# Kernel optimization log

Measured on AMD Instinct MI355X. Metric: run time of the kernel, lower is better.

## Reference

```python
import jax, jax.numpy as jnp
import numpy as np

DIM = 1024
HEADS = 16
HEAD_DIM = DIM // HEADS
EPS = 1e-6


def rmsnorm(x, w):
    var = jnp.mean(x * x, axis=-1, keepdims=True)
    return x * jax.lax.rsqrt(var + EPS) * w


def setup_inputs() -> dict:
    key = jax.random.key(0)
    ks = jax.random.split(key, 8)
    B, N, M = 2, 2048, 512
    s = 1.0 / np.sqrt(DIM)
    return {
        "x": jax.random.normal(ks[0], (B, N, DIM), jnp.float32),
        "context": jax.random.normal(ks[1], (B, M, DIM), jnp.float32),
        "qkv_w": jax.random.normal(ks[2], (3 * DIM, DIM), jnp.float32) * s,
        "kv_y_w": jax.random.normal(ks[3], (2 * DIM, DIM), jnp.float32) * s,
        "proj_w": jax.random.normal(ks[4], (DIM, DIM), jnp.float32) * s,
        "proj_b": jnp.zeros((DIM,), jnp.float32),
        "q_norm_w": jnp.ones((HEAD_DIM,), jnp.float32),
        "k_norm_w": jnp.ones((HEAD_DIM,), jnp.float32),
    }


def reference(x, context, qkv_w, kv_y_w, proj_w, proj_b, q_norm_w, k_norm_w):
    B, N, C = x.shape
    H, D = HEADS, HEAD_DIM
    scale = D ** -0.5
    qkv = (x @ qkv_w.T).reshape(B, N, 3, H, D).transpose(2, 0, 3, 1, 4)
    q, kx, vx = qkv[0], qkv[1], qkv[2]
    q = rmsnorm(q, q_norm_w)
    kx = rmsnorm(kx, k_norm_w)
    M = context.shape[1]
    kv = (context @ kv_y_w.T).reshape(B, M, 2, H, D).transpose(2, 0, 3, 1, 4)
    ky, vy = kv[0], kv[1]
    ky = rmsnorm(ky, k_norm_w)
    k = jnp.concatenate([kx, ky], axis=2)  # [B,H,N+M,D]
    v = jnp.concatenate([vx, vy], axis=2)
    attn = jax.nn.softmax(jnp.einsum("bhnd,bhmd->bhnm", q, k) * scale, axis=-1)
    out = jnp.einsum("bhnm,bhmd->bhnd", attn, v).transpose(0, 2, 1, 3).reshape(B, N, C)
    return out @ proj_w.T + proj_b
```

## Files before the change

### kernel.cpp

```cpp
#include <hip/hip_runtime.h>
#include <hip/hip_bf16.h>
#include <stdint.h>

#define DEVINL __device__ __forceinline__

typedef unsigned short u16;
typedef unsigned int u32;
typedef __attribute__((ext_vector_type(8))) __bf16 bf16x8;
typedef __attribute__((ext_vector_type(4))) float f32x4;
typedef __attribute__((ext_vector_type(16))) float f32x16;

static constexpr int NQ = 2048, MC = 512, DIMC = 1024, LTOT = 2560;
static constexpr float EPS = 1e-6f;

DEVINL u16 f2bf(float f) {
  u32 u = __float_as_uint(f);
  u32 r = (u + 0x7FFFu + ((u >> 16) & 1u)) >> 16;
  return (u16)r;
}
DEVINL float bf2f(u16 h) { return __uint_as_float(((u32)h) << 16); }

DEVINL void gload16(const void* g, void* l) {
  __builtin_amdgcn_global_load_lds((const __attribute__((address_space(1))) void*)g,
                                   (__attribute__((address_space(3))) void*)l, 16, 0, 0);
}

__global__ void cvt_all(const float* __restrict__ x, const float* __restrict__ ctx,
                        const float* __restrict__ w1, const float* __restrict__ w2,
                        const float* __restrict__ w3,
                        u16* __restrict__ xb, u16* __restrict__ cb, u16* __restrict__ wq,
                        u16* __restrict__ wk, u16* __restrict__ wp) {
  const int bk = blockIdx.x;
  const float* src; u16* dst; int lb;
  if (bk < 2048)      { src = x;   dst = xb; lb = bk; }
  else if (bk < 2560) { src = ctx; dst = cb; lb = bk - 2048; }
  else if (bk < 4096) { src = w1;  dst = wq; lb = bk - 2560; }
  else if (bk < 5120) { src = w2;  dst = wk; lb = bk - 4096; }
  else                { src = w3;  dst = wp; lb = bk - 5120; }
  size_t i = ((size_t)lb * 256 + threadIdx.x) * 8;
  float4 a = *(const float4*)(src + i);
  float4 b = *(const float4*)(src + i + 4);
  union { uint4 u; u16 s[8]; } o;
  o.s[0] = f2bf(a.x); o.s[1] = f2bf(a.y); o.s[2] = f2bf(a.z); o.s[3] = f2bf(a.w);
  o.s[4] = f2bf(b.x); o.s[5] = f2bf(b.y); o.s[6] = f2bf(b.z); o.s[7] = f2bf(b.w);
  *(uint4*)(dst + i) = o.u;
}

template <int M, int N, int K, bool OUT_BF16, bool HAS_BIAS>
__launch_bounds__(256, 2)
__global__ void gemm_bt(const u16* __restrict__ A, const u16* __restrict__ Bw,
                        void* __restrict__ Cout, const float* __restrict__ bias) {
  __shared__ u16 la[128 * 64];
  __shared__ u16 lb[128 * 64];
  const int tid = threadIdx.x;
  const int lane = tid & 63, wid = tid >> 6;
  const int tm = blockIdx.x / (N / 128), tn = blockIdx.x % (N / 128);
  const int m0 = tm * 128, n0 = tn * 128;
  const int wm = (wid >> 1) * 64, wn = (wid & 1) * 64;
  const int srow = lane >> 3, scol = (lane & 7) * 8;
  const int cn = lane & 15, rg = lane >> 4;

  f32x4 acc[4][4] = {};

  for (int kt = 0; kt < K; kt += 64) {
    __syncthreads();
#pragma unroll
    for (int c = 0; c < 4; ++c) {
      int s = c * 4 + wid;
      gload16(A + (size_t)(m0 + s * 8 + srow) * K + kt + scol, &la[s * 512]);
      gload16(Bw + (size_t)(n0 + s * 8 + srow) * K + kt + scol, &lb[s * 512]);
    }
    __syncthreads();
#pragma unroll
    for (int kk = 0; kk < 2; ++kk) {
      bf16x8 af[4], bfr[4];
      const int ko = kk * 32 + rg * 8;
#pragma unroll
      for (int mi = 0; mi < 4; ++mi) af[mi] = *(const bf16x8*)&la[(wm + mi * 16 + cn) * 64 + ko];
#pragma unroll
      for (int ni = 0; ni < 4; ++ni) bfr[ni] = *(const bf16x8*)&lb[(wn + ni * 16 + cn) * 64 + ko];
#pragma unroll
      for (int mi = 0; mi < 4; ++mi)
#pragma unroll
        for (int ni = 0; ni < 4; ++ni)
          acc[mi][ni] = __builtin_amdgcn_mfma_f32_16x16x32_bf16(af[mi], bfr[ni], acc[mi][ni], 0, 0, 0);
    }
  }
#pragma unroll
  for (int mi = 0; mi < 4; ++mi)
#pragma unroll
    for (int ni = 0; ni < 4; ++ni) {
      const int col = n0 + wn + ni * 16 + cn;
      const float bv = HAS_BIAS ? bias[col] : 0.0f;
#pragma unroll
      for (int r = 0; r < 4; ++r) {
        const int row = m0 + wm + mi * 16 + rg * 4 + r;
        const float v = acc[mi][ni][r] + bv;
        if (OUT_BF16) ((u16*)Cout)[(size_t)row * N + col] = f2bf(v);
        else          ((float*)Cout)[(size_t)row * N + col] = v;
      }
    }
}

__global__ void reorg_kv(const u16* __restrict__ qkvx, const u16* __restrict__ kvy,
                         const float* __restrict__ knw,
                         u16* __restrict__ kfb, u16* __restrict__ vfb) {
  __shared__ u16 lk[64 * 72];
  const int tid = threadIdx.x;
  const int bh = blockIdx.x / 40, g = blockIdx.x % 40;
  const int b = bh >> 4, h = bh & 15;
  const u16* src; int stride, kcol, vcol, srow0;
  if (g < 32) {
    src = qkvx; stride = 3 * DIMC; kcol = DIMC + h * 64; vcol = 2 * DIMC + h * 64;
    srow0 = b * NQ + g * 64;
  } else {
    src = kvy; stride = 2 * DIMC; kcol = h * 64; vcol = DIMC + h * 64;
    srow0 = b * MC + (g - 32) * 64;
  }
  {
    const int i = tid >> 2, d0 = (tid & 3) * 16;
    const u16* p = src + (size_t)(srow0 + i) * stride + kcol + d0;
    uint4 r0 = *(const uint4*)(p);
    uint4 r1 = *(const uint4*)(p + 8);
    const u16* s0 = (const u16*)&r0; const u16* s1 = (const u16*)&r1;
    float f[16]; float ss = 0.f;
#pragma unroll
    for (int j = 0; j < 8; ++j) { f[j] = bf2f(s0[j]); ss += f[j] * f[j]; }
#pragma unroll
    for (int j = 0; j < 8; ++j) { f[8 + j] = bf2f(s1[j]); ss += f[8 + j] * f[8 + j]; }
    ss += __shfl_xor(ss, 1); ss += __shfl_xor(ss, 2);
    const float rs = rsqrtf(ss * (1.0f / 64.0f) + EPS);
    union { uint4 u; u16 s[8]; } o0, o1;
#pragma unroll
    for (int j = 0; j < 8; ++j) o0.s[j] = f2bf(f[j] * rs * knw[d0 + j]);
#pragma unroll
    for (int j = 0; j < 8; ++j) o1.s[j] = f2bf(f[8 + j] * rs * knw[d0 + 8 + j]);
    *(uint4*)&lk[i * 72 + d0] = o0.u;
    *(uint4*)&lk[i * 72 + d0 + 8] = o1.u;
  }
  __syncthreads();
#pragma unroll
  for (int c0 = 0; c0 < 512; c0 += 256) {
    const int c = c0 + tid;
    const int l = c & 63, s = (c >> 6) & 3, tt = c >> 8;
    const int ln32 = l & 31, hi = l >> 5;
    const size_t tbase = ((size_t)bh * 80 + g * 2 + tt) * 2048;
    uint4 kv4 = *(const uint4*)&lk[(tt * 32 + ln32) * 72 + s * 16 + hi * 8];
    *(uint4*)(kfb + tbase + s * 512 + l * 8) = kv4;
    const int key = tt * 32 + (s & 1) * 16 + hi * 8;
    const int d = (s >> 1) * 32 + ln32;
    const u16* vp = src + (size_t)(srow0 + key) * stride + vcol + d;
    union { uint4 u; u16 e[8]; } t;
#pragma unroll
    for (int j = 0; j < 8; ++j) t.e[j] = vp[(size_t)j * stride];
    *(uint4*)(vfb + tbase + s * 512 + l * 8) = t.u;
  }
}

__launch_bounds__(256, 4)
__global__ void attn_fwd(const u16* __restrict__ qkvx, const u16* __restrict__ kfb,
                         const u16* __restrict__ vfb, const float* __restrict__ qnw,
                         u16* __restrict__ pacc, float* __restrict__ mlb) {
  const int tid = threadIdx.x;
  const int lane = tid & 63, wid = tid >> 6;
  const int hi = lane >> 5, ln32 = lane & 31;
  const int swz = (blockIdx.x & 7) * 128 + (blockIdx.x >> 3);
  const int sp = swz & 1, qt = (swz >> 1) & 15, bh = swz >> 5;
  const int b = bh >> 4, h = bh & 15;
  const int qrow = qt * 128 + wid * 32 + ln32;

  union U4 { uint4 u; bf16x8 v; };

  bf16x8 qb[4];
  {
    const u16* qp = qkvx + (size_t)(b * NQ + qrow) * (3 * DIMC) + h * 64 + hi * 8;
    uint4 qr4[4];
#pragma unroll
    for (int s = 0; s < 4; ++s) qr4[s] = *(const uint4*)(qp + s * 16);
    float f[32]; float ss = 0.f;
#pragma unroll
    for (int s = 0; s < 4; ++s) {
      const u16* e = (const u16*)&qr4[s];
#pragma unroll
      for (int j = 0; j < 8; ++j) { float v = bf2f(e[j]); f[s * 8 + j] = v; ss += v * v; }
    }
    ss += __shfl_xor(ss, 32);
    const float rs = rsqrtf(ss * (1.0f / 64.0f) + EPS) * 0.125f * 1.44269504088896f;
#pragma unroll
    for (int s = 0; s < 4; ++s) {
      union { u16 s16[8]; bf16x8 v; } o;
#pragma unroll
      for (int j = 0; j < 8; ++j) o.s16[j] = f2bf(f[s * 8 + j] * rs * qnw[s * 16 + hi * 8 + j]);
      qb[s] = o.v;
    }
  }

  const u16* kbase = kfb + ((size_t)bh * 80 + sp * 40) * 2048 + lane * 8;
  const u16* vbase = vfb + ((size_t)bh * 80 + sp * 40) * 2048 + lane * 8;

  U4 kf[4];
#pragma unroll
  for (int s = 0; s < 4; ++s) kf[s].u = *(const uint4*)(kbase + s * 512);

  float m_run = -1e30f, l_run = 0.f;
  f32x16 acc0 = {}, acc1 = {};

#pragma unroll 2
  for (int t = 0; t < 40; ++t) {
    const u16* vt = vbase + (size_t)t * 2048;
    U4 vf[4];
#pragma unroll
    for (int vi = 0; vi < 4; ++vi) vf[vi].u = *(const uint4*)(vt + vi * 512);

    f32x16 sa = {};
#pragma unroll
    for (int s = 0; s < 4; ++s)
      sa = __builtin_amdgcn_mfma_f32_32x32x16_bf16(kf[s].v, qb[s], sa, 0, 0, 0);

    const u16* kt = kbase + (size_t)(t + 1) * 2048;
    U4 kn[4];
#pragma unroll
    for (int s = 0; s < 4; ++s) kn[s].u = *(const uint4*)(kt + s * 512);

    float t8[8];
#pragma unroll
    for (int j = 0; j < 8; ++j) t8[j] = fmaxf(sa[j], sa[j + 8]);
    float t4m[4];
#pragma unroll
    for (int j = 0; j < 4; ++j) t4m[j] = fmaxf(t8[j], t8[j + 4]);
    float mx = fmaxf(fmaxf(t4m[0], t4m[2]), fmaxf(t4m[1], t4m[3]));
    mx = fmaxf(mx, __shfl_xor(mx, 32));
    if (__any(mx > m_run + 8.0f)) {
      const float mn = fmaxf(m_run, mx);
      const float corr = exp2f(m_run - mn);
      m_run = mn;
      l_run *= corr;
#pragma unroll
      for (int r = 0; r < 16; ++r) {
        const int qr = (r & 3) + 8 * (r >> 2) + 4 * hi;
        const float c = __shfl(corr, qr);
        acc0[r] *= c; acc1[r] *= c;
      }
    }
    float p[16];
#pragma unroll
    for (int r = 0; r < 16; ++r) p[r] = exp2f(sa[r] - m_run);
    float s8[8];
#pragma unroll
    for (int j = 0; j < 8; ++j) s8[j] = p[j] + p[j + 8];
    float s4[4];
#pragma unroll
    for (int j = 0; j < 4; ++j) s4[j] = s8[j] + s8[j + 4];
    float sum = (s4[0] + s4[2]) + (s4[1] + s4[3]);
    sum += __shfl_xor(sum, 32);
    l_run += sum;

    u32 w[8];
#pragma unroll
    for (int j = 0; j < 8; ++j) {
      __hip_bfloat162 h2 = __float22bfloat162_rn(make_float2(p[2 * j], p[2 * j + 1]));
      w[j] = *(u32*)&h2;
    }
    union { u32 w4[4]; bf16x8 v; } pa0, pa1;
#pragma unroll
    for (int g = 0; g < 2; ++g)
#pragma unroll
      for (int j = 0; j < 2; ++j) {
        const u32 a = w[4 * g + j], c = w[4 * g + j + 2];
        const u32 xa = __shfl_xor(a, 32), xc = __shfl_xor(c, 32);
        u32 lo_w = hi ? xc : a;
        u32 hi_w = hi ? c : xa;
        if (g == 0) { pa0.w4[j] = lo_w; pa0.w4[j + 2] = hi_w; }
        else        { pa1.w4[j] = lo_w; pa1.w4[j + 2] = hi_w; }
      }

    acc0 = __builtin_amdgcn_mfma_f32_32x32x16_bf16(pa0.v, vf[0].v, acc0, 0, 0, 0);
    acc0 = __builtin_amdgcn_mfma_f32_32x32x16_bf16(pa1.v, vf[1].v, acc0, 0, 0, 0);
    acc1 = __builtin_amdgcn_mfma_f32_32x32x16_bf16(pa0.v, vf[2].v, acc1, 0, 0, 0);
    acc1 = __builtin_amdgcn_mfma_f32_32x32x16_bf16(pa1.v, vf[3].v, acc1, 0, 0, 0);

#pragma unroll
    for (int s = 0; s < 4; ++s) kf[s] = kn[s];
  }

  const float rinv = 1.0f / l_run;
  u16* po = pacc + (size_t)sp * 4194304 +
            (size_t)(b * NQ + qt * 128 + wid * 32) * DIMC + h * 64 + ln32;
#pragma unroll
  for (int r = 0; r < 16; ++r) {
    const int qr = (r & 3) + 8 * (r >> 2) + 4 * hi;
    const float ri = __shfl(rinv, qr);
    po[(size_t)qr * DIMC] = f2bf(acc0[r] * ri);
    po[(size_t)qr * DIMC + 32] = f2bf(acc1[r] * ri);
  }
  if (lane < 32) {
    const int mlidx = (b * NQ + qt * 128 + wid * 32 + ln32) * 16 + h;
    mlb[(sp * 2 + 0) * 65536 + mlidx] = m_run;
    mlb[(sp * 2 + 1) * 65536 + mlidx] = l_run;
  }
}

__global__ void attn_combine(const u16* __restrict__ pacc, const float* __restrict__ mlb,
                             u16* __restrict__ attnb) {
  const int g = blockIdx.x * 256 + threadIdx.x;
  const int combo = g >> 3, dc = (g & 7) * 8;
  const float m0 = mlb[combo],             l0 = mlb[65536 + combo];
  const float m1 = mlb[2 * 65536 + combo], l1 = mlb[3 * 65536 + combo];
  const float m = fmaxf(m0, m1);
  const float w0 = l0 * exp2f(m0 - m), w1 = l1 * exp2f(m1 - m);
  const float rinv = 1.0f / (w0 + w1);
  const int row = combo >> 4, h = combo & 15;
  const size_t off = (size_t)row * DIMC + h * 64 + dc;
  uint4 a0 = *(const uint4*)(pacc + off);
  uint4 a1 = *(const uint4*)(pacc + 4194304 + off);
  const u16* p0 = (const u16*)&a0; const u16* p1 = (const u16*)&a1;
  union { uint4 u; u16 s[8]; } o;
#pragma unroll
  for (int j = 0; j < 8; ++j)
    o.s[j] = f2bf((w0 * bf2f(p0[j]) + w1 * bf2f(p1[j])) * rinv);
  *(uint4*)(attnb + off) = o.u;
}

extern "C" void kernel_launch(void* const* d_in, const int* in_sizes, int n_in,
                              void* d_out, int out_size, void* d_ws, size_t ws_size,
                              hipStream_t stream) {
  const float* x      = (const float*)d_in[0];
  const float* ctx    = (const float*)d_in[1];
  const float* qkv_w  = (const float*)d_in[2];
  const float* kv_y_w = (const float*)d_in[3];
  const float* proj_w = (const float*)d_in[4];
  const float* proj_b = (const float*)d_in[5];
  const float* q_norm_w = (const float*)d_in[6];
  const float* k_norm_w = (const float*)d_in[7];
  float* out = (float*)d_out;

  char* ws = (char*)d_ws;
  u16* xb    = (u16*)(ws);
  u16* cb    = (u16*)(ws + 8388608);
  u16* wqkv  = (u16*)(ws + 10485760);
  u16* wkv   = (u16*)(ws + 16777216);
  u16* wproj = (u16*)(ws + 20971520);
  u16* qkvx  = (u16*)(ws + 23068672);
  u16* kvy   = (u16*)(ws + 48234496);
  u16* kfb   = (u16*)(ws + 52428800);
  u16* vfb   = (u16*)(ws + 62914560);
  u16* attnb = (u16*)(ws + 73400320);
  u16*   pacc = (u16*)(ws);
  float* mlb  = (float*)(ws + 16777216);

  cvt_all<<<5632, 256, 0, stream>>>(x, ctx, qkv_w, kv_y_w, proj_w, xb, cb, wqkv, wkv, wproj);

  gemm_bt<4096, 3072, 1024, true, false><<<32 * 24, 256, 0, stream>>>(xb, wqkv, qkvx, nullptr);
  gemm_bt<1024, 2048, 1024, true, false><<<8 * 16, 256, 0, stream>>>(cb, wkv, kvy, nullptr);
  reorg_kv<<<32 * 40, 256, 0, stream>>>(qkvx, kvy, k_norm_w, kfb, vfb);
  attn_fwd<<<1024, 256, 0, stream>>>(qkvx, kfb, vfb, q_norm_w, pacc, mlb);
  attn_combine<<<2048, 256, 0, stream>>>(pacc, mlb, attnb);
  gemm_bt<4096, 1024, 1024, false, true><<<32 * 8, 256, 0, stream>>>(attnb, wproj, out, proj_b);
}
```

Before: 271.4 us.

## Add BM-templated GEMM tiles and restructure attention inner loop with MFMA row sums

The GEMM is templated on its M tile size so the small KV-context GEMM and the output projection run with 64-row tiles, launching more blocks to fill the GPU. The attention loop is reworked in several ways: K fragments double-buffer without copies, the max reduction is flattened, and the cross-half P shuffle uses v_permlane32_swap. MFMA sections are given raised s_setprio priority. The softmax denominator is now accumulated by an extra MFMA against a vector of ones instead of scalar adds and shuffles, which adds matrix work and bf16-rounded row sums in exchange for fewer VALU ops.

```diff
diff --git a/kernel.cpp b/kernel.cpp
--- a/kernel.cpp
+++ b/kernel.cpp
@@ -46,48 +46,53 @@
   *(uint4*)(dst + i) = o.u;
 }
 
-template <int M, int N, int K, bool OUT_BF16, bool HAS_BIAS>
+template <int BM, int M, int N, int K, bool OUT_BF16, bool HAS_BIAS>
 __launch_bounds__(256, 2)
 __global__ void gemm_bt(const u16* __restrict__ A, const u16* __restrict__ Bw,
                         void* __restrict__ Cout, const float* __restrict__ bias) {
-  __shared__ u16 la[128 * 64];
+  constexpr int MI = BM / 32;
+  __shared__ u16 la[BM * 64];
   __shared__ u16 lb[128 * 64];
   const int tid = threadIdx.x;
   const int lane = tid & 63, wid = tid >> 6;
   const int tm = blockIdx.x / (N / 128), tn = blockIdx.x % (N / 128);
-  const int m0 = tm * 128, n0 = tn * 128;
-  const int wm = (wid >> 1) * 64, wn = (wid & 1) * 64;
+  const int m0 = tm * BM, n0 = tn * 128;
+  const int wm = (wid >> 1) * (BM / 2), wn = (wid & 1) * 64;
   const int srow = lane >> 3, scol = (lane & 7) * 8;
   const int cn = lane & 15, rg = lane >> 4;
 
-  f32x4 acc[4][4] = {};
+  f32x4 acc[MI][4] = {};
 
   for (int kt = 0; kt < K; kt += 64) {
     __syncthreads();
 #pragma unroll
+    for (int c = 0; c < MI; ++c) {
+      int s = c * 4 + wid;
+      gload16(A + (size_t)(m0 + s * 8 + srow) * K + kt + scol, &la[s * 512]);
+    }
+#pragma unroll
     for (int c = 0; c < 4; ++c) {
       int s = c * 4 + wid;
-      gload16(A + (size_t)(m0 + s * 8 + srow) * K + kt + scol, &la[s * 512]);
       gload16(Bw + (size_t)(n0 + s * 8 + srow) * K + kt + scol, &lb[s * 512]);
     }
     __syncthreads();
 #pragma unroll
     for (int kk = 0; kk < 2; ++kk) {
-      bf16x8 af[4], bfr[4];
+      bf16x8 af[MI], bfr[4];
       const int ko = kk * 32 + rg * 8;
 #pragma unroll
-      for (int mi = 0; mi < 4; ++mi) af[mi] = *(const bf16x8*)&la[(wm + mi * 16 + cn) * 64 + ko];
+      for (int mi = 0; mi < MI; ++mi) af[mi] = *(const bf16x8*)&la[(wm + mi * 16 + cn) * 64 + ko];
 #pragma unroll
       for (int ni = 0; ni < 4; ++ni) bfr[ni] = *(const bf16x8*)&lb[(wn + ni * 16 + cn) * 64 + ko];
 #pragma unroll
-      for (int mi = 0; mi < 4; ++mi)
+      for (int mi = 0; mi < MI; ++mi)
 #pragma unroll
         for (int ni = 0; ni < 4; ++ni)
           acc[mi][ni] = __builtin_amdgcn_mfma_f32_16x16x32_bf16(af[mi], bfr[ni], acc[mi][ni], 0, 0, 0);
     }
   }
 #pragma unroll
-  for (int mi = 0; mi < 4; ++mi)
+  for (int mi = 0; mi < MI; ++mi)
 #pragma unroll
     for (int ni = 0; ni < 4; ++ni) {
       const int col = n0 + wn + ni * 16 + cn;
@@ -198,62 +203,54 @@
   const u16* kbase = kfb + ((size_t)bh * 80 + sp * 40) * 2048 + lane * 8;
   const u16* vbase = vfb + ((size_t)bh * 80 + sp * 40) * 2048 + lane * 8;
 
-  U4 kf[4];
-#pragma unroll
-  for (int s = 0; s < 4; ++s) kf[s].u = *(const uint4*)(kbase + s * 512);
-
-  float m_run = -1e30f, l_run = 0.f;
-  f32x16 acc0 = {}, acc1 = {};
-
-#pragma unroll 2
-  for (int t = 0; t < 40; ++t) {
+  U4 kfA[4], kfB[4];
+#pragma unroll
+  for (int s = 0; s < 4; ++s) kfA[s].u = *(const uint4*)(kbase + s * 512);
+
+  union { u32 w4[4]; bf16x8 v; } ones;
+  ones.w4[0] = ones.w4[1] = ones.w4[2] = ones.w4[3] = 0x3F803F80u;
+
+  float m_run = -1e30f;
+  f32x16 acc0 = {}, acc1 = {}, accl = {};
+
+  auto step = [&](U4 (&kc)[4], U4 (&kn)[4], int t) {
     const u16* vt = vbase + (size_t)t * 2048;
     U4 vf[4];
 #pragma unroll
     for (int vi = 0; vi < 4; ++vi) vf[vi].u = *(const uint4*)(vt + vi * 512);
 
+    __builtin_amdgcn_s_setprio(1);
     f32x16 sa = {};
 #pragma unroll
     for (int s = 0; s < 4; ++s)
-      sa = __builtin_amdgcn_mfma_f32_32x32x16_bf16(kf[s].v, qb[s], sa, 0, 0, 0);
-
-    const u16* kt = kbase + (size_t)(t + 1) * 2048;
-    U4 kn[4];
-#pragma unroll
-    for (int s = 0; s < 4; ++s) kn[s].u = *(const uint4*)(kt + s * 512);
-
-    float t8[8];
-#pragma unroll
-    for (int j = 0; j < 8; ++j) t8[j] = fmaxf(sa[j], sa[j + 8]);
-    float t4m[4];
-#pragma unroll
-    for (int j = 0; j < 4; ++j) t4m[j] = fmaxf(t8[j], t8[j + 4]);
-    float mx = fmaxf(fmaxf(t4m[0], t4m[2]), fmaxf(t4m[1], t4m[3]));
+      sa = __builtin_amdgcn_mfma_f32_32x32x16_bf16(kc[s].v, qb[s], sa, 0, 0, 0);
+    __builtin_amdgcn_s_setprio(0);
+
+    const u16* kp = kbase + (size_t)(t + 1) * 2048;
+#pragma unroll
+    for (int s = 0; s < 4; ++s) kn[s].u = *(const uint4*)(kp + s * 512);
+
+    float x0 = fmaxf(fmaxf(sa[0], sa[1]), sa[2]);
+    float x1 = fmaxf(fmaxf(sa[3], sa[4]), sa[5]);
+    float x2 = fmaxf(fmaxf(sa[6], sa[7]), sa[8]);
+    float x3 = fmaxf(fmaxf(sa[9], sa[10]), sa[11]);
+    float x4 = fmaxf(fmaxf(sa[12], sa[13]), sa[14]);
+    float mx = fmaxf(fmaxf(fmaxf(x0, x1), x2), fmaxf(fmaxf(x3, x4), sa[15]));
     mx = fmaxf(mx, __shfl_xor(mx, 32));
     if (__any(mx > m_run + 8.0f)) {
       const float mn = fmaxf(m_run, mx);
       const float corr = exp2f(m_run - mn);
       m_run = mn;
-      l_run *= corr;
 #pragma unroll
       for (int r = 0; r < 16; ++r) {
         const int qr = (r & 3) + 8 * (r >> 2) + 4 * hi;
         const float c = __shfl(corr, qr);
-        acc0[r] *= c; acc1[r] *= c;
+        acc0[r] *= c; acc1[r] *= c; accl[r] *= c;
       }
     }
     float p[16];
 #pragma unroll
     for (int r = 0; r < 16; ++r) p[r] = exp2f(sa[r] - m_run);
-    float s8[8];
-#pragma unroll
-    for (int j = 0; j < 8; ++j) s8[j] = p[j] + p[j + 8];
-    float s4[4];
-#pragma unroll
-    for (int j = 0; j < 4; ++j) s4[j] = s8[j] + s8[j + 4];
-    float sum = (s4[0] + s4[2]) + (s4[1] + s4[3]);
-    sum += __shfl_xor(sum, 32);
-    l_run += sum;
 
     u32 w[8];
 #pragma unroll
@@ -262,41 +259,56 @@
       w[j] = *(u32*)&h2;
     }
     union { u32 w4[4]; bf16x8 v; } pa0, pa1;
-#pragma unroll
-    for (int g = 0; g < 2; ++g)
-#pragma unroll
-      for (int j = 0; j < 2; ++j) {
-        const u32 a = w[4 * g + j], c = w[4 * g + j + 2];
-        const u32 xa = __shfl_xor(a, 32), xc = __shfl_xor(c, 32);
-        u32 lo_w = hi ? xc : a;
-        u32 hi_w = hi ? c : xa;
-        if (g == 0) { pa0.w4[j] = lo_w; pa0.w4[j + 2] = hi_w; }
-        else        { pa1.w4[j] = lo_w; pa1.w4[j + 2] = hi_w; }
-      }
-
+    {
+      u32 a, c;
+      a = w[0]; c = w[2];
+      asm("v_permlane32_swap_b32 %0, %1" : "+v"(a), "+v"(c));
+      pa0.w4[0] = a; pa0.w4[2] = c;
+      a = w[1]; c = w[3];
+      asm("v_permlane32_swap_b32 %0, %1" : "+v"(a), "+v"(c));
+      pa0.w4[1] = a; pa0.w4[3] = c;
+      a = w[4]; c = w[6];
+      asm("v_permlane32_swap_b32 %0, %1" : "+v"(a), "+v"(c));
+      pa1.w4[0] = a; pa1.w4[2] = c;
+      a = w[5]; c = w[7];
+      asm("v_permlane32_swap_b32 %0, %1" : "+v"(a), "+v"(c));
+      pa1.w4[1] = a; pa1.w4[3] = c;
+    }
+
+    __builtin_amdgcn_s_setprio(1);
     acc0 = __builtin_amdgcn_mfma_f32_32x32x16_bf16(pa0.v, vf[0].v, acc0, 0, 0, 0);
     acc0 = __builtin_amdgcn_mfma_f32_32x32x16_bf16(pa1.v, vf[1].v, acc0, 0, 0, 0);
     acc1 = __builtin_amdgcn_mfma_f32_32x32x16_bf16(pa0.v, vf[2].v, acc1, 0, 0, 0);
     acc1 = __builtin_amdgcn_mfma_f32_32x32x16_bf16(pa1.v, vf[3].v, acc1, 0, 0, 0);
-
-#pragma unroll
-    for (int s = 0; s < 4; ++s) kf[s] = kn[s];
-  }
-
-  const float rinv = 1.0f / l_run;
+    accl = __builtin_amdgcn_mfma_f32_32x32x16_bf16(pa0.v, ones.v, accl, 0, 0, 0);
+    accl = __builtin_amdgcn_mfma_f32_32x32x16_bf16(pa1.v, ones.v, accl, 0, 0, 0);
+    __builtin_amdgcn_s_setprio(0);
+  };
+
+#pragma unroll 1
+  for (int t = 0; t < 40; t += 2) {
+    step(kfA, kfB, t);
+    step(kfB, kfA, t + 1);
+  }
+
   u16* po = pacc + (size_t)sp * 4194304 +
             (size_t)(b * NQ + qt * 128 + wid * 32) * DIMC + h * 64 + ln32;
 #pragma unroll
   for (int r = 0; r < 16; ++r) {
     const int qr = (r & 3) + 8 * (r >> 2) + 4 * hi;
-    const float ri = __shfl(rinv, qr);
+    const float ri = 1.0f / accl[r];
     po[(size_t)qr * DIMC] = f2bf(acc0[r] * ri);
     po[(size_t)qr * DIMC + 32] = f2bf(acc1[r] * ri);
   }
   if (lane < 32) {
-    const int mlidx = (b * NQ + qt * 128 + wid * 32 + ln32) * 16 + h;
-    mlb[(sp * 2 + 0) * 65536 + mlidx] = m_run;
-    mlb[(sp * 2 + 1) * 65536 + mlidx] = l_run;
+    mlb[(sp * 2 + 0) * 65536 + (b * NQ + qt * 128 + wid * 32 + ln32) * 16 + h] = m_run;
+  }
+  if (ln32 == 0) {
+#pragma unroll
+    for (int r = 0; r < 16; ++r) {
+      const int qr = (r & 3) + 8 * (r >> 2) + 4 * hi;
+      mlb[(sp * 2 + 1) * 65536 + (b * NQ + qt * 128 + wid * 32 + qr) * 16 + h] = accl[r];
+    }
   }
 }
 
@@ -350,10 +362,10 @@
 
   cvt_all<<<5632, 256, 0, stream>>>(x, ctx, qkv_w, kv_y_w, proj_w, xb, cb, wqkv, wkv, wproj);
 
-  gemm_bt<4096, 3072, 1024, true, false><<<32 * 24, 256, 0, stream>>>(xb, wqkv, qkvx, nullptr);
-  gemm_bt<1024, 2048, 1024, true, false><<<8 * 16, 256, 0, stream>>>(cb, wkv, kvy, nullptr);
+  gemm_bt<128, 4096, 3072, 1024, true, false><<<32 * 24, 256, 0, stream>>>(xb, wqkv, qkvx, nullptr);
+  gemm_bt<64, 1024, 2048, 1024, true, false><<<16 * 16, 256, 0, stream>>>(cb, wkv, kvy, nullptr);
   reorg_kv<<<32 * 40, 256, 0, stream>>>(qkvx, kvy, k_norm_w, kfb, vfb);
   attn_fwd<<<1024, 256, 0, stream>>>(qkvx, kfb, vfb, q_norm_w, pacc, mlb);
   attn_combine<<<2048, 256, 0, stream>>>(pacc, mlb, attnb);
-  gemm_bt<4096, 1024, 1024, false, true><<<32 * 8, 256, 0, stream>>>(attnb, wproj, out, proj_b);
-}
+  gemm_bt<64, 4096, 1024, 1024, false, true><<<64 * 8, 256, 0, stream>>>(attnb, wproj, out, proj_b);
+}
```

New measurement: 293.7 us. 1.08x slower.
